# Kernel optimization log

Hardware: AMD Instinct MI355X
Metric: run time of the kernel (lower is better)

Reference implementation:

```python
import jax, jax.numpy as jnp
import numpy as np

D = 1024
H = 16
DH = D // H  # 64
EPS_LN = 1e-5
CONF_MIN = 1e-6


def sparsemax(z):
    """Sparsemax along the last axis (Martins & Astudillo 2016)."""
    K = z.shape[-1]
    z_sorted = jnp.flip(jnp.sort(z, axis=-1), axis=-1)          # descending
    cssv = jnp.cumsum(z_sorted, axis=-1)                        # cumulative sums
    r = jnp.arange(1, K + 1, dtype=z.dtype)                     # 1..K
    support = (1.0 + r * z_sorted) > cssv                       # bool mask
    k = jnp.sum(support, axis=-1, keepdims=True)                # support size
    tau = (jnp.take_along_axis(cssv, k.astype(jnp.int32) - 1, axis=-1) - 1.0) / k.astype(z.dtype)
    return jnp.maximum(z - tau, 0.0)


def setup_inputs() -> dict:
    key = jax.random.key(0)
    ks = jax.random.split(key, 16)
    B, P, K = 8, 512, 16
    s = 0.02
    return {
        "cell_query": jax.random.normal(ks[0], (B, D), jnp.float32),
        "gene_facets": jax.random.normal(ks[1], (B, P, K, D), jnp.float32),
        "confidence": jax.random.uniform(ks[2], (B, P, K), jnp.float32),
        "wq": jax.random.normal(ks[3], (D, D), jnp.float32) * s,
        "bq": jnp.zeros((D,), jnp.float32),
        "wk": jax.random.normal(ks[4], (D, D), jnp.float32) * s,
        "bk": jnp.zeros((D,), jnp.float32),
        "wv": jax.random.normal(ks[5], (D, D), jnp.float32) * s,
        "bv": jnp.zeros((D,), jnp.float32),
        "wo": jax.random.normal(ks[6], (D, D), jnp.float32) * s,
        "bo": jnp.zeros((D,), jnp.float32),
        "gamma": jnp.ones((D,), jnp.float32),
        "beta": jnp.zeros((D,), jnp.float32),
    }


def reference(cell_query, gene_facets, confidence,
              wq, bq, wk, bk, wv, bv, wo, bo, gamma, beta):
    B = gene_facets.shape[0]
    P = gene_facets.shape[1]
    Kf = gene_facets.shape[2]

    # Projections (torch Linear: x @ W^T + b; here weights stored already transposed as (D,D))
    Q = (cell_query @ wq + bq).reshape(B, H, DH)                       # (B,H,d)
    Kp = (gene_facets @ wk + bk).reshape(B, P, Kf, H, DH)              # (B,P,K,H,d)
    Vp = (gene_facets @ wv + bv).reshape(B, P, Kf, H, DH)              # (B,P,K,H,d)

    # scores: (B,P,H,K)
    scores = jnp.einsum('bhd,bpkhd->bphk', Q, Kp) / jnp.sqrt(jnp.asarray(DH, Q.dtype))
    conf_bias = jnp.log(jnp.clip(confidence, CONF_MIN))                # (B,P,K)
    scores = scores + conf_bias[:, :, None, :]

    alpha = sparsemax(scores)                                          # (B,P,H,K), dropout_p=0 -> identity

    out = jnp.einsum('bphk,bpkhd->bphd', alpha, Vp).reshape(B, P, D)
    out = out @ wo + bo

    # LayerNorm over last dim
    mu = jnp.mean(out, axis=-1, keepdims=True)
    var = jnp.mean((out - mu) ** 2, axis=-1, keepdims=True)
    out = (out - mu) * jax.lax.rsqrt(var + EPS_LN) * gamma + beta
    return out, alpha
```

## Files before the change

### kernel.cpp

```cpp
#include <hip/hip_runtime.h>


typedef float f32x4 __attribute__((ext_vector_type(4)));
typedef short s16x4 __attribute__((ext_vector_type(4)));
typedef short s16x8 __attribute__((ext_vector_type(8)));

__device__ __forceinline__ unsigned short f2bf(float f) {
  unsigned u = __builtin_bit_cast(unsigned, f);
  u = (u + 0x7FFFu + ((u >> 16) & 1u)) >> 16;
  return (unsigned short)u;
}

__device__ __forceinline__ s16x8 pack8(s16x4 lo, s16x4 hi) {
  s16x8 r;
  r[0] = lo[0]; r[1] = lo[1]; r[2] = lo[2]; r[3] = lo[3];
  r[4] = hi[0]; r[5] = hi[1]; r[6] = hi[2]; r[7] = hi[3];
  return r;
}

__global__ __launch_bounds__(256) void k_trans(
    const float* __restrict__ wv, const float* __restrict__ wo,
    unsigned short* __restrict__ wvt, unsigned short* __restrict__ wot) {
  __shared__ float ts[64][65];
  int bid = blockIdx.x;
  const float* src = (bid < 256) ? wv : wo;
  unsigned short* dst = (bid < 256) ? wvt : wot;
  int tile = bid & 255;
  int er = (tile >> 4) << 6;
  int cb = (tile & 15) << 6;
  int t = threadIdx.x;
  int r = t >> 2, c0 = (t & 3) << 4;
#pragma unroll
  for (int j = 0; j < 16; j += 4) {
    f32x4 v = *(const f32x4*)&src[(long)(er + r) * 1024 + cb + c0 + j];
    ts[r][c0 + j + 0] = v[0];
    ts[r][c0 + j + 1] = v[1];
    ts[r][c0 + j + 2] = v[2];
    ts[r][c0 + j + 3] = v[3];
  }
  __syncthreads();
  s16x8 o0, o1;
#pragma unroll
  for (int j = 0; j < 8; ++j) o0[j] = (short)f2bf(ts[c0 + j][r]);
#pragma unroll
  for (int j = 0; j < 8; ++j) o1[j] = (short)f2bf(ts[c0 + 8 + j][r]);
  long ob = (long)(cb + r) * 1024 + er + c0;
  *(s16x8*)&dst[ob] = o0;
  *(s16x8*)&dst[ob + 8] = o1;
}

__global__ __launch_bounds__(256) void k_qpart(
    const float* __restrict__ cq, const float* __restrict__ wq,
    float* __restrict__ qpart) {
  int eq = blockIdx.x, b = blockIdx.y, t = threadIdx.x;
  int d0 = t << 2;
  f32x4 acc = {0.f, 0.f, 0.f, 0.f};
#pragma unroll 4
  for (int i = 0; i < 64; ++i) {
    int e = (eq << 6) + i;
    float c = cq[(b << 10) + e];
    f32x4 w = *(const f32x4*)&wq[(long)e * 1024 + d0];
    acc += w * c;
  }
  *(f32x4*)&qpart[(long)((b << 4) + eq) * 1024 + d0] = acc;
}

__global__ __launch_bounds__(256) void k_wtilde(
    const float* __restrict__ wk, const float* __restrict__ bk,
    const float* __restrict__ bq, const float* __restrict__ qpart,
    unsigned short* __restrict__ wt, float* __restrict__ cvec) {
  __shared__ float Qs[16][68];
  int et = blockIdx.x, b = blockIdx.y, t = threadIdx.x;
#pragma unroll
  for (int j = 0; j < 4; ++j) {
    int d = t + (j << 8);
    float s = bq[d];
    for (int q = 0; q < 16; ++q) s += qpart[(long)((b << 4) + q) * 1024 + d];
    Qs[d >> 6][d & 63] = s;
  }
  __syncthreads();
  int h = t & 15, el = t >> 4;
#pragma unroll
  for (int ii = 0; ii < 8; ++ii) {
    int e = (et << 7) + (ii << 4) + el;
    const float* wr = &wk[(long)e * 1024 + (h << 6)];
    float s = 0.f;
#pragma unroll
    for (int d = 0; d < 64; d += 4) {
      f32x4 w = *(const f32x4*)&wr[d];
      s += w[0] * Qs[h][d] + w[1] * Qs[h][d + 1] + w[2] * Qs[h][d + 2] + w[3] * Qs[h][d + 3];
    }
    wt[(long)((b << 4) + h) * 1024 + e] = f2bf(s);
  }
  if (et == 0 && t < 16) {
    float s = 0.f;
    for (int d = 0; d < 64; ++d) s += bk[(t << 6) + d] * Qs[t][d];
    cvec[(b << 4) + t] = s;
  }
}

#define GSTR 1028
__global__ __launch_bounds__(256, 2) void k_scores(
    const float* __restrict__ G, const float* __restrict__ conf,
    const unsigned short* __restrict__ wt, const float* __restrict__ cvec,
    float* __restrict__ alpha_out, unsigned short* __restrict__ gbar, int b0) {
  __shared__ short smem[33408];
  __shared__ float fsm[1040];
  short* Gs = smem;
  short* Ws = smem + 16 * GSTR;
  short* As = smem + 32 * GSTR;
  float* ps = fsm;
  float* lc = fsm + 1024;

  int t = threadIdx.x;
  int lane = t & 63, w = t >> 6;
  int bp = blockIdx.x;
  long gbp = (long)b0 * 512 + bp;
  int b = (int)(gbp >> 9);
  const float* Grow = G + gbp * 16384;
  const unsigned short* wtb = wt + (long)b * 16384;

#pragma unroll
  for (int it = 0; it < 8; ++it) {
    int flat = (it << 11) + (t << 3);
    s16x8 v = *(const s16x8*)&wtb[flat];
    short* dst = &Ws[(flat >> 10) * GSTR + (flat & 1023)];
    *(s16x4*)dst = (s16x4){v[0], v[1], v[2], v[3]};
    *(s16x4*)(dst + 4) = (s16x4){v[4], v[5], v[6], v[7]};
  }
  if (t < 32) {
    short* base = (t < 16) ? Gs : Ws;
    *(s16x4*)&base[(t & 15) * GSTR + 1024] = (s16x4){0, 0, 0, 0};
  }
  if (t < 16) lc[t] = logf(fmaxf(conf[gbp * 16 + t], 1e-6f));

#pragma unroll
  for (int k = 0; k < 16; ++k) {
    f32x4 g = *(const f32x4*)&Grow[(k << 10) + (t << 2)];
    s16x4 h4;
    h4[0] = (short)f2bf(g[0]); h4[1] = (short)f2bf(g[1]);
    h4[2] = (short)f2bf(g[2]); h4[3] = (short)f2bf(g[3]);
    *(s16x4*)&Gs[k * GSTR + (t << 2)] = h4;
  }
  __syncthreads();

  int l15 = lane & 15, g4 = lane >> 4;
  f32x4 sc = {0.f, 0.f, 0.f, 0.f};
#pragma unroll
  for (int i = 0; i < 8; ++i) {
    int eb = (w << 8) + (i << 5) + (g4 << 3);
    int off = l15 * GSTR + eb;
    s16x8 avf = pack8(*(const s16x4*)&Ws[off], *(const s16x4*)&Ws[off + 4]);
    s16x8 bvf = pack8(*(const s16x4*)&Gs[off], *(const s16x4*)&Gs[off + 4]);
    sc = __builtin_amdgcn_mfma_f32_16x16x32_bf16(avf, bvf, sc, 0, 0, 0);
  }
#pragma unroll
  for (int r = 0; r < 4; ++r)
    ps[(w << 8) + ((g4 << 2) + r) * 16 + l15] = sc[r];
  __syncthreads();

  int h = t >> 4, k = t & 15;
  float z = (ps[h * 16 + k] + ps[256 + h * 16 + k] + ps[512 + h * 16 + k] +
             ps[768 + h * 16 + k] + cvec[b * 16 + h]) * 0.125f + lc[k];
  float v = z;
#pragma unroll
  for (int kk = 2; kk <= 16; kk <<= 1) {
#pragma unroll
    for (int j = kk >> 1; j > 0; j >>= 1) {
      float o = __shfl_xor(v, j, 64);
      bool dirDesc = ((l15 & kk) == 0);
      bool takeMax = (((l15 & j) == 0) == dirDesc);
      v = takeMax ? fmaxf(v, o) : fminf(v, o);
    }
  }
  float cs = v;
#pragma unroll
  for (int d = 1; d < 16; d <<= 1) {
    float o = __shfl_up(cs, (unsigned)d, 16);
    if (l15 >= d) cs += o;
  }
  bool sup = (1.0f + (float)(l15 + 1) * v) > cs;
  unsigned long long m = __ballot(sup);
  int gb16 = lane & 48;
  int ksup = (int)__popcll((m >> gb16) & 0xFFFFull);
  float csk = __shfl(cs, ksup - 1, 16);
  float tau = (csk - 1.0f) / (float)ksup;
  float a = fmaxf(z - tau, 0.0f);
  alpha_out[((gbp << 4) + h) * 16 + k] = a;
  As[(h << 5) + k] = (short)f2bf(a);
  As[(h << 5) + 16 + k] = 0;
  __syncthreads();

  s16x8 ab = *(const s16x8*)&As[(l15 << 5) + (g4 << 3)];
  unsigned short* gbo = gbar + ((long)bp << 14);
#pragma unroll 4
  for (int i = 0; i < 16; ++i) {
    int ebase = ((w << 4) + i) << 4;
    int eA = ebase + l15;
    s16x8 aa;
#pragma unroll
    for (int j = 0; j < 8; ++j) aa[j] = Gs[((g4 << 3) + j) * GSTR + eA];
    f32x4 d2 = __builtin_amdgcn_mfma_f32_16x16x32_bf16(
        aa, ab, (f32x4){0.f, 0.f, 0.f, 0.f}, 0, 0, 0);
    s16x4 o4;
    o4[0] = (short)f2bf(d2[0]); o4[1] = (short)f2bf(d2[1]);
    o4[2] = (short)f2bf(d2[2]); o4[3] = (short)f2bf(d2[3]);
    *(s16x4*)&gbo[(l15 << 10) + ebase + (g4 << 2)] = o4;
  }
}

__global__ __launch_bounds__(256) void k_av(
    const unsigned short* __restrict__ gbar, const unsigned short* __restrict__ wvt,
    const float* __restrict__ bv, unsigned short* __restrict__ av, int b0) {
  __shared__ short Asm[64 * 40];
  __shared__ short Bsm[64 * 40];
  int tile = blockIdx.x, h = blockIdx.y, t = threadIdx.x;
  int lane = t & 63, w = t >> 6;
  int wm = w >> 1, wn = w & 1;
  int l15 = lane & 15, g4 = lane >> 4;
  f32x4 acc[2][2] = {};
  int lr = t >> 2, ls = (t & 3) << 3;
  const unsigned short* Ar = gbar + ((long)(tile * 64 + lr)) * 16384 + h * 1024;
  const unsigned short* Br = wvt + ((long)((h << 6) + lr)) * 1024;
  s16x8 a8 = *(const s16x8*)&Ar[ls];
  s16x8 b8 = *(const s16x8*)&Br[ls];
  for (int kb = 0; kb < 32; ++kb) {
    __syncthreads();
    *(s16x8*)&Asm[lr * 40 + ls] = a8;
    *(s16x8*)&Bsm[lr * 40 + ls] = b8;
    if (kb + 1 < 32) {
      a8 = *(const s16x8*)&Ar[((kb + 1) << 5) + ls];
      b8 = *(const s16x8*)&Br[((kb + 1) << 5) + ls];
    }
    __syncthreads();
    s16x8 afr[2], bfr[2];
#pragma unroll
    for (int im = 0; im < 2; ++im)
      afr[im] = *(const s16x8*)&Asm[(wm * 32 + im * 16 + l15) * 40 + (g4 << 3)];
#pragma unroll
    for (int in = 0; in < 2; ++in)
      bfr[in] = *(const s16x8*)&Bsm[(wn * 32 + in * 16 + l15) * 40 + (g4 << 3)];
#pragma unroll
    for (int im = 0; im < 2; ++im)
#pragma unroll
      for (int in = 0; in < 2; ++in)
        acc[im][in] = __builtin_amdgcn_mfma_f32_16x16x32_bf16(afr[im], bfr[in], acc[im][in], 0, 0, 0);
  }
#pragma unroll
  for (int in = 0; in < 2; ++in) {
    int colg = (h << 6) + wn * 32 + in * 16 + l15;
    float bvv = bv[colg];
#pragma unroll
    for (int im = 0; im < 2; ++im) {
      long rowg = (long)b0 * 512 + tile * 64 + wm * 32 + im * 16 + (g4 << 2);
#pragma unroll
      for (int r = 0; r < 4; ++r)
        av[(rowg + r) * 1024 + colg] = f2bf(acc[im][in][r] + bvv);
    }
  }
}

__global__ __launch_bounds__(256) void k_out(
    const unsigned short* __restrict__ av, const unsigned short* __restrict__ wot,
    const float* __restrict__ bo, float* __restrict__ y) {
  __shared__ short Asm[128 * 40];
  __shared__ short Bsm[128 * 40];
  int mt = blockIdx.x, nt = blockIdx.y, t = threadIdx.x;
  int lane = t & 63, w = t >> 6;
  int wm = w >> 1, wn = w & 1;
  int l15 = lane & 15, g4 = lane >> 4;
  f32x4 acc[4][4] = {};
  int lr = t >> 1, ls = (t & 1) << 4;
  const unsigned short* Ar = av + ((long)(mt * 128 + lr)) * 1024;
  const unsigned short* Br = wot + ((long)(nt * 128 + lr)) * 1024;
  s16x8 a0 = *(const s16x8*)&Ar[ls];
  s16x8 a1 = *(const s16x8*)&Ar[ls + 8];
  s16x8 b0 = *(const s16x8*)&Br[ls];
  s16x8 b1 = *(const s16x8*)&Br[ls + 8];
  for (int kb = 0; kb < 32; ++kb) {
    __syncthreads();
    short* pa = &Asm[lr * 40 + ls];
    *(s16x8*)pa = a0; *(s16x8*)(pa + 8) = a1;
    short* pb = &Bsm[lr * 40 + ls];
    *(s16x8*)pb = b0; *(s16x8*)(pb + 8) = b1;
    if (kb + 1 < 32) {
      a0 = *(const s16x8*)&Ar[((kb + 1) << 5) + ls];
      a1 = *(const s16x8*)&Ar[((kb + 1) << 5) + ls + 8];
      b0 = *(const s16x8*)&Br[((kb + 1) << 5) + ls];
      b1 = *(const s16x8*)&Br[((kb + 1) << 5) + ls + 8];
    }
    __syncthreads();
    s16x8 afr[4], bfr[4];
#pragma unroll
    for (int im = 0; im < 4; ++im)
      afr[im] = *(const s16x8*)&Asm[(wm * 64 + im * 16 + l15) * 40 + (g4 << 3)];
#pragma unroll
    for (int in = 0; in < 4; ++in)
      bfr[in] = *(const s16x8*)&Bsm[(wn * 64 + in * 16 + l15) * 40 + (g4 << 3)];
#pragma unroll
    for (int im = 0; im < 4; ++im)
#pragma unroll
      for (int in = 0; in < 4; ++in)
        acc[im][in] = __builtin_amdgcn_mfma_f32_16x16x32_bf16(afr[im], bfr[in], acc[im][in], 0, 0, 0);
  }
#pragma unroll
  for (int in = 0; in < 4; ++in) {
    int colg = nt * 128 + wn * 64 + in * 16 + l15;
    float bov = bo[colg];
#pragma unroll
    for (int im = 0; im < 4; ++im) {
      long rowg = mt * 128 + wm * 64 + im * 16 + (g4 << 2);
#pragma unroll
      for (int r = 0; r < 4; ++r)
        y[(rowg + r) * 1024 + colg] = acc[im][in][r] + bov;
    }
  }
}

__global__ __launch_bounds__(256) void k_ln(
    float* __restrict__ y, const float* __restrict__ gamma,
    const float* __restrict__ beta) {
  int row = (blockIdx.x << 2) + (threadIdx.x >> 6);
  int lane = threadIdx.x & 63;
  float* yr = y + ((long)row << 10);
  f32x4 v[4];
  float s = 0.f, s2 = 0.f;
#pragma unroll
  for (int j = 0; j < 4; ++j) {
    v[j] = *(const f32x4*)&yr[(lane << 2) + (j << 8)];
#pragma unroll
    for (int q = 0; q < 4; ++q) { s += v[j][q]; s2 += v[j][q] * v[j][q]; }
  }
#pragma unroll
  for (int d = 1; d < 64; d <<= 1) {
    s += __shfl_xor(s, d, 64);
    s2 += __shfl_xor(s2, d, 64);
  }
  float mu = s * (1.0f / 1024.0f);
  float var = s2 * (1.0f / 1024.0f) - mu * mu;
  float rs = rsqrtf(var + 1e-5f);
#pragma unroll
  for (int j = 0; j < 4; ++j) {
    int f0 = (lane << 2) + (j << 8);
    f32x4 gm = *(const f32x4*)&gamma[f0];
    f32x4 bt = *(const f32x4*)&beta[f0];
    f32x4 o;
#pragma unroll
    for (int q = 0; q < 4; ++q) o[q] = (v[j][q] - mu) * rs * gm[q] + bt[q];
    *(f32x4*)&yr[f0] = o;
  }
}

extern "C" void kernel_launch(void* const* d_in, const int* in_sizes, int n_in,
                              void* d_out, int out_size, void* d_ws, size_t ws_size,
                              hipStream_t stream) {
  (void)in_sizes; (void)n_in; (void)out_size;
  const float* cq    = (const float*)d_in[0];
  const float* G     = (const float*)d_in[1];
  const float* conf  = (const float*)d_in[2];
  const float* wq    = (const float*)d_in[3];
  const float* bq    = (const float*)d_in[4];
  const float* wk    = (const float*)d_in[5];
  const float* bk    = (const float*)d_in[6];
  const float* wv    = (const float*)d_in[7];
  const float* bv    = (const float*)d_in[8];
  const float* wo    = (const float*)d_in[9];
  const float* bo    = (const float*)d_in[10];
  const float* gamma = (const float*)d_in[11];
  const float* beta  = (const float*)d_in[12];

  float* y = (float*)d_out;
  float* alpha = y + 4194304;

  char* p = (char*)d_ws;
  float* qpart = (float*)p;                 p += 8L * 16 * 1024 * 4;
  float* cvec  = (float*)p;                 p += 1024;
  unsigned short* wt   = (unsigned short*)p; p += 8L * 16 * 1024 * 2;
  unsigned short* wvt  = (unsigned short*)p; p += 1024L * 1024 * 2;
  unsigned short* wot  = (unsigned short*)p; p += 1024L * 1024 * 2;
  unsigned short* av   = (unsigned short*)p; p += 4096L * 1024 * 2;
  unsigned short* gbar = (unsigned short*)p;
  size_t used = (size_t)(p - (char*)d_ws);
  size_t per_b = 512L * 16 * 1024 * 2;
  int nb = 1;
  if (ws_size >= used + 8 * per_b) nb = 8;
  else if (ws_size >= used + 4 * per_b) nb = 4;
  else if (ws_size >= used + 2 * per_b) nb = 2;

  hipLaunchKernelGGL(k_trans, dim3(512), dim3(256), 0, stream, wv, wo, wvt, wot);
  hipLaunchKernelGGL(k_qpart, dim3(16, 8), dim3(256), 0, stream, cq, wq, qpart);
  hipLaunchKernelGGL(k_wtilde, dim3(8, 8), dim3(256), 0, stream, wk, bk, bq, qpart, wt, cvec);
  for (int c = 0; c < 8; c += nb) {
    hipLaunchKernelGGL(k_scores, dim3(nb * 512), dim3(256), 0, stream,
                       G, conf, wt, cvec, alpha, gbar, c);
    hipLaunchKernelGGL(k_av, dim3(nb * 8, 16), dim3(256), 0, stream,
                       gbar, wvt, bv, av, c);
  }
  hipLaunchKernelGGL(k_out, dim3(32, 8), dim3(256), 0, stream, av, wot, bo, y);
  hipLaunchKernelGGL(k_ln, dim3(1024), dim3(256), 0, stream, y, gamma, beta);
}
```

Baseline: 232.2 us.

## Transpose gbar to head-major, stage transposed G tile, enlarge k_av tiles

k_scores now builds a transposed bf16 copy of the G tile in shared memory, so the second MFMA reads contiguous vectors instead of eight strided scalar LDS loads. It reads the W-tilde fragments straight from global memory rather than staging them in LDS. gbar is written head-major (head stride passed as a parameter) so k_av reads contiguous rows, and k_av now uses 128-row tiles, launching half as many blocks. k_qpart computes all 8 batches in one block per weight slice, so wq is read once instead of eight times. The extra LDS for Gt raises shared-memory use, which may cut k_scores occupancy.

```diff
diff --git a/kernel.cpp b/kernel.cpp
--- a/kernel.cpp
+++ b/kernel.cpp
@@ -52,17 +52,18 @@
 __global__ __launch_bounds__(256) void k_qpart(
     const float* __restrict__ cq, const float* __restrict__ wq,
     float* __restrict__ qpart) {
-  int eq = blockIdx.x, b = blockIdx.y, t = threadIdx.x;
+  int eq = blockIdx.x, t = threadIdx.x;
   int d0 = t << 2;
-  f32x4 acc = {0.f, 0.f, 0.f, 0.f};
-#pragma unroll 4
+  f32x4 acc[8] = {};
   for (int i = 0; i < 64; ++i) {
     int e = (eq << 6) + i;
-    float c = cq[(b << 10) + e];
     f32x4 w = *(const f32x4*)&wq[(long)e * 1024 + d0];
-    acc += w * c;
-  }
-  *(f32x4*)&qpart[(long)((b << 4) + eq) * 1024 + d0] = acc;
+#pragma unroll
+    for (int b = 0; b < 8; ++b) acc[b] += w * cq[(b << 10) + e];
+  }
+#pragma unroll
+  for (int b = 0; b < 8; ++b)
+    *(f32x4*)&qpart[(long)((b << 4) + eq) * 1024 + d0] = acc[b];
 }
 
 __global__ __launch_bounds__(256) void k_wtilde(
@@ -100,20 +101,21 @@
 }
 
 #define GSTR 1028
+#define TSTR 20
 __global__ __launch_bounds__(256, 2) void k_scores(
     const float* __restrict__ G, const float* __restrict__ conf,
     const unsigned short* __restrict__ wt, const float* __restrict__ cvec,
-    float* __restrict__ alpha_out, unsigned short* __restrict__ gbar, int b0) {
-  __shared__ short smem[33408];
-  __shared__ float fsm[1040];
-  short* Gs = smem;
-  short* Ws = smem + 16 * GSTR;
-  short* As = smem + 32 * GSTR;
-  float* ps = fsm;
-  float* lc = fsm + 1024;
+    float* __restrict__ alpha_out, unsigned short* __restrict__ gbar,
+    int b0, int hstride) {
+  __shared__ short Gs[16 * GSTR];
+  __shared__ short Gt[1024 * TSTR];
+  __shared__ short As[16 * 32];
+  __shared__ float ps[1024];
+  __shared__ float lc[16];
 
   int t = threadIdx.x;
   int lane = t & 63, w = t >> 6;
+  int l15 = lane & 15, g4 = lane >> 4;
   int bp = blockIdx.x;
   long gbp = (long)b0 * 512 + bp;
   int b = (int)(gbp >> 9);
@@ -121,138 +123,147 @@
   const unsigned short* wtb = wt + (long)b * 16384;
 
 #pragma unroll
-  for (int it = 0; it < 8; ++it) {
-    int flat = (it << 11) + (t << 3);
-    s16x8 v = *(const s16x8*)&wtb[flat];
-    short* dst = &Ws[(flat >> 10) * GSTR + (flat & 1023)];
-    *(s16x4*)dst = (s16x4){v[0], v[1], v[2], v[3]};
-    *(s16x4*)(dst + 4) = (s16x4){v[4], v[5], v[6], v[7]};
-  }
-  if (t < 32) {
-    short* base = (t < 16) ? Gs : Ws;
-    *(s16x4*)&base[(t & 15) * GSTR + 1024] = (s16x4){0, 0, 0, 0};
+  for (int half = 0; half < 2; ++half) {
+    s16x4 col[8];
+#pragma unroll
+    for (int j = 0; j < 8; ++j) {
+      int k = (half << 3) + j;
+      f32x4 g = *(const f32x4*)&Grow[(k << 10) + (t << 2)];
+      s16x4 h4;
+      h4[0] = (short)f2bf(g[0]); h4[1] = (short)f2bf(g[1]);
+      h4[2] = (short)f2bf(g[2]); h4[3] = (short)f2bf(g[3]);
+      *(s16x4*)&Gs[k * GSTR + (t << 2)] = h4;
+      col[j] = h4;
+    }
+#pragma unroll
+    for (int q = 0; q < 4; ++q) {
+      int e = (t << 2) + q;
+      s16x4 lo, hi;
+      lo[0] = col[0][q]; lo[1] = col[1][q]; lo[2] = col[2][q]; lo[3] = col[3][q];
+      hi[0] = col[4][q]; hi[1] = col[5][q]; hi[2] = col[6][q]; hi[3] = col[7][q];
+      *(s16x4*)&Gt[e * TSTR + (half << 3)] = lo;
+      *(s16x4*)&Gt[e * TSTR + (half << 3) + 4] = hi;
+    }
   }
   if (t < 16) lc[t] = logf(fmaxf(conf[gbp * 16 + t], 1e-6f));
-
-#pragma unroll
-  for (int k = 0; k < 16; ++k) {
-    f32x4 g = *(const f32x4*)&Grow[(k << 10) + (t << 2)];
-    s16x4 h4;
-    h4[0] = (short)f2bf(g[0]); h4[1] = (short)f2bf(g[1]);
-    h4[2] = (short)f2bf(g[2]); h4[3] = (short)f2bf(g[3]);
-    *(s16x4*)&Gs[k * GSTR + (t << 2)] = h4;
-  }
   __syncthreads();
 
-  int l15 = lane & 15, g4 = lane >> 4;
   f32x4 sc = {0.f, 0.f, 0.f, 0.f};
 #pragma unroll
   for (int i = 0; i < 8; ++i) {
-    int eb = (w << 8) + (i << 5) + (g4 << 3);
-    int off = l15 * GSTR + eb;
-    s16x8 avf = pack8(*(const s16x4*)&Ws[off], *(const s16x4*)&Ws[off + 4]);
-    s16x8 bvf = pack8(*(const s16x4*)&Gs[off], *(const s16x4*)&Gs[off + 4]);
-    sc = __builtin_amdgcn_mfma_f32_16x16x32_bf16(avf, bvf, sc, 0, 0, 0);
+    int e0 = (w << 8) + (i << 5) + (g4 << 3);
+    s16x8 af = *(const s16x8*)&wtb[l15 * 1024 + e0];
+    int off = l15 * GSTR + e0;
+    s16x8 bf = pack8(*(const s16x4*)&Gs[off], *(const s16x4*)&Gs[off + 4]);
+    sc = __builtin_amdgcn_mfma_f32_16x16x32_bf16(af, bf, sc, 0, 0, 0);
   }
 #pragma unroll
   for (int r = 0; r < 4; ++r)
     ps[(w << 8) + ((g4 << 2) + r) * 16 + l15] = sc[r];
   __syncthreads();
 
-  int h = t >> 4, k = t & 15;
-  float z = (ps[h * 16 + k] + ps[256 + h * 16 + k] + ps[512 + h * 16 + k] +
-             ps[768 + h * 16 + k] + cvec[b * 16 + h]) * 0.125f + lc[k];
-  float v = z;
-#pragma unroll
-  for (int kk = 2; kk <= 16; kk <<= 1) {
-#pragma unroll
-    for (int j = kk >> 1; j > 0; j >>= 1) {
-      float o = __shfl_xor(v, j, 64);
-      bool dirDesc = ((l15 & kk) == 0);
-      bool takeMax = (((l15 & j) == 0) == dirDesc);
-      v = takeMax ? fmaxf(v, o) : fminf(v, o);
-    }
-  }
-  float cs = v;
-#pragma unroll
-  for (int d = 1; d < 16; d <<= 1) {
-    float o = __shfl_up(cs, (unsigned)d, 16);
-    if (l15 >= d) cs += o;
-  }
-  bool sup = (1.0f + (float)(l15 + 1) * v) > cs;
-  unsigned long long m = __ballot(sup);
-  int gb16 = lane & 48;
-  int ksup = (int)__popcll((m >> gb16) & 0xFFFFull);
-  float csk = __shfl(cs, ksup - 1, 16);
-  float tau = (csk - 1.0f) / (float)ksup;
-  float a = fmaxf(z - tau, 0.0f);
-  alpha_out[((gbp << 4) + h) * 16 + k] = a;
-  As[(h << 5) + k] = (short)f2bf(a);
-  As[(h << 5) + 16 + k] = 0;
+  {
+    int h = t >> 4, k = t & 15;
+    float z = (ps[h * 16 + k] + ps[256 + h * 16 + k] + ps[512 + h * 16 + k] +
+               ps[768 + h * 16 + k] + cvec[b * 16 + h]) * 0.125f + lc[k];
+    float v = z;
+#pragma unroll
+    for (int kk = 2; kk <= 16; kk <<= 1) {
+#pragma unroll
+      for (int j = kk >> 1; j > 0; j >>= 1) {
+        float o = __shfl_xor(v, j, 64);
+        bool dirDesc = ((l15 & kk) == 0);
+        bool takeMax = (((l15 & j) == 0) == dirDesc);
+        v = takeMax ? fmaxf(v, o) : fminf(v, o);
+      }
+    }
+    float cs = v;
+#pragma unroll
+    for (int d = 1; d < 16; d <<= 1) {
+      float o = __shfl_up(cs, (unsigned)d, 16);
+      if (l15 >= d) cs += o;
+    }
+    bool sup = (1.0f + (float)(l15 + 1) * v) > cs;
+    unsigned long long m = __ballot(sup);
+    int gb16 = lane & 48;
+    int ksup = (int)__popcll((m >> gb16) & 0xFFFFull);
+    float csk = __shfl(cs, ksup - 1, 16);
+    float tau = (csk - 1.0f) / (float)ksup;
+    float a = fmaxf(z - tau, 0.0f);
+    alpha_out[((gbp << 4) + h) * 16 + k] = a;
+    As[(h << 5) + k] = (short)f2bf(a);
+    As[(h << 5) + 16 + k] = 0;
+  }
   __syncthreads();
 
   s16x8 ab = *(const s16x8*)&As[(l15 << 5) + (g4 << 3)];
-  unsigned short* gbo = gbar + ((long)bp << 14);
 #pragma unroll 4
   for (int i = 0; i < 16; ++i) {
     int ebase = ((w << 4) + i) << 4;
-    int eA = ebase + l15;
-    s16x8 aa;
-#pragma unroll
-    for (int j = 0; j < 8; ++j) aa[j] = Gs[((g4 << 3) + j) * GSTR + eA];
+    int ro = (ebase + l15) * TSTR + ((g4 & 1) << 3);
+    s16x8 aa = pack8(*(const s16x4*)&Gt[ro], *(const s16x4*)&Gt[ro + 4]);
     f32x4 d2 = __builtin_amdgcn_mfma_f32_16x16x32_bf16(
         aa, ab, (f32x4){0.f, 0.f, 0.f, 0.f}, 0, 0, 0);
     s16x4 o4;
     o4[0] = (short)f2bf(d2[0]); o4[1] = (short)f2bf(d2[1]);
     o4[2] = (short)f2bf(d2[2]); o4[3] = (short)f2bf(d2[3]);
-    *(s16x4*)&gbo[(l15 << 10) + ebase + (g4 << 2)] = o4;
+    *(s16x4*)&gbar[(long)l15 * hstride + (long)bp * 1024 + ebase + (g4 << 2)] = o4;
   }
 }
 
 __global__ __launch_bounds__(256) void k_av(
     const unsigned short* __restrict__ gbar, const unsigned short* __restrict__ wvt,
-    const float* __restrict__ bv, unsigned short* __restrict__ av, int b0) {
-  __shared__ short Asm[64 * 40];
+    const float* __restrict__ bv, unsigned short* __restrict__ av,
+    int b0, int hstride) {
+  __shared__ short Asm[128 * 40];
   __shared__ short Bsm[64 * 40];
-  int tile = blockIdx.x, h = blockIdx.y, t = threadIdx.x;
+  int t = threadIdx.x;
   int lane = t & 63, w = t >> 6;
+  int l15 = lane & 15, g4 = lane >> 4;
   int wm = w >> 1, wn = w & 1;
-  int l15 = lane & 15, g4 = lane >> 4;
-  f32x4 acc[2][2] = {};
-  int lr = t >> 2, ls = (t & 3) << 3;
-  const unsigned short* Ar = gbar + ((long)(tile * 64 + lr)) * 16384 + h * 1024;
-  const unsigned short* Br = wvt + ((long)((h << 6) + lr)) * 1024;
-  s16x8 a8 = *(const s16x8*)&Ar[ls];
-  s16x8 b8 = *(const s16x8*)&Br[ls];
+  int tile = blockIdx.x, h = blockIdx.y;
+  const unsigned short* Ab = gbar + (long)h * hstride + (long)tile * 128 * 1024;
+  const unsigned short* Bb = wvt + (long)(h << 6) * 1024;
+  int ar = t >> 1, ac = (t & 1) << 4;
+  int br = t >> 2, bc = (t & 3) << 3;
+  const unsigned short* Arp = Ab + (long)ar * 1024 + ac;
+  const unsigned short* Brp = Bb + (long)br * 1024 + bc;
+  s16x8 a0 = *(const s16x8*)&Arp[0];
+  s16x8 a1 = *(const s16x8*)&Arp[8];
+  s16x8 b8 = *(const s16x8*)&Brp[0];
+  f32x4 acc[4][2] = {};
   for (int kb = 0; kb < 32; ++kb) {
     __syncthreads();
-    *(s16x8*)&Asm[lr * 40 + ls] = a8;
-    *(s16x8*)&Bsm[lr * 40 + ls] = b8;
+    short* pa = &Asm[ar * 40 + ac];
+    *(s16x8*)pa = a0; *(s16x8*)(pa + 8) = a1;
+    *(s16x8*)&Bsm[br * 40 + bc] = b8;
     if (kb + 1 < 32) {
-      a8 = *(const s16x8*)&Ar[((kb + 1) << 5) + ls];
-      b8 = *(const s16x8*)&Br[((kb + 1) << 5) + ls];
+      a0 = *(const s16x8*)&Arp[((kb + 1) << 5)];
+      a1 = *(const s16x8*)&Arp[((kb + 1) << 5) + 8];
+      b8 = *(const s16x8*)&Brp[((kb + 1) << 5)];
     }
     __syncthreads();
-    s16x8 afr[2], bfr[2];
-#pragma unroll
-    for (int im = 0; im < 2; ++im)
-      afr[im] = *(const s16x8*)&Asm[(wm * 32 + im * 16 + l15) * 40 + (g4 << 3)];
+    s16x8 afr[4], bfr[2];
+#pragma unroll
+    for (int im = 0; im < 4; ++im)
+      afr[im] = *(const s16x8*)&Asm[(wm * 64 + im * 16 + l15) * 40 + (g4 << 3)];
 #pragma unroll
     for (int in = 0; in < 2; ++in)
       bfr[in] = *(const s16x8*)&Bsm[(wn * 32 + in * 16 + l15) * 40 + (g4 << 3)];
 #pragma unroll
-    for (int im = 0; im < 2; ++im)
+    for (int im = 0; im < 4; ++im)
 #pragma unroll
       for (int in = 0; in < 2; ++in)
         acc[im][in] = __builtin_amdgcn_mfma_f32_16x16x32_bf16(afr[im], bfr[in], acc[im][in], 0, 0, 0);
   }
+  long grow0 = (long)b0 * 512 + (long)tile * 128 + wm * 64 + (g4 << 2);
 #pragma unroll
   for (int in = 0; in < 2; ++in) {
     int colg = (h << 6) + wn * 32 + in * 16 + l15;
     float bvv = bv[colg];
 #pragma unroll
-    for (int im = 0; im < 2; ++im) {
-      long rowg = (long)b0 * 512 + tile * 64 + wm * 32 + im * 16 + (g4 << 2);
+    for (int im = 0; im < 4; ++im) {
+      long rowg = grow0 + im * 16;
 #pragma unroll
       for (int r = 0; r < 4; ++r)
         av[(rowg + r) * 1024 + colg] = f2bf(acc[im][in][r] + bvv);
@@ -373,8 +384,8 @@
   float* alpha = y + 4194304;
 
   char* p = (char*)d_ws;
-  float* qpart = (float*)p;                 p += 8L * 16 * 1024 * 4;
-  float* cvec  = (float*)p;                 p += 1024;
+  float* qpart = (float*)p;                  p += 8L * 16 * 1024 * 4;
+  float* cvec  = (float*)p;                  p += 1024;
   unsigned short* wt   = (unsigned short*)p; p += 8L * 16 * 1024 * 2;
   unsigned short* wvt  = (unsigned short*)p; p += 1024L * 1024 * 2;
   unsigned short* wot  = (unsigned short*)p; p += 1024L * 1024 * 2;
@@ -386,15 +397,16 @@
   if (ws_size >= used + 8 * per_b) nb = 8;
   else if (ws_size >= used + 4 * per_b) nb = 4;
   else if (ws_size >= used + 2 * per_b) nb = 2;
+  int hstride = nb * 512 * 1024;
 
   hipLaunchKernelGGL(k_trans, dim3(512), dim3(256), 0, stream, wv, wo, wvt, wot);
-  hipLaunchKernelGGL(k_qpart, dim3(16, 8), dim3(256), 0, stream, cq, wq, qpart);
+  hipLaunchKernelGGL(k_qpart, dim3(16), dim3(256), 0, stream, cq, wq, qpart);
   hipLaunchKernelGGL(k_wtilde, dim3(8, 8), dim3(256), 0, stream, wk, bk, bq, qpart, wt, cvec);
   for (int c = 0; c < 8; c += nb) {
     hipLaunchKernelGGL(k_scores, dim3(nb * 512), dim3(256), 0, stream,
-                       G, conf, wt, cvec, alpha, gbar, c);
-    hipLaunchKernelGGL(k_av, dim3(nb * 8, 16), dim3(256), 0, stream,
-                       gbar, wvt, bv, av, c);
+                       G, conf, wt, cvec, alpha, gbar, c, hstride);
+    hipLaunchKernelGGL(k_av, dim3(nb * 4, 16), dim3(256), 0, stream,
+                       gbar, wvt, bv, av, c, hstride);
   }
   hipLaunchKernelGGL(k_out, dim3(32, 8), dim3(256), 0, stream, av, wot, bo, y);
   hipLaunchKernelGGL(k_ln, dim3(1024), dim3(256), 0, stream, y, gamma, beta);
```

After: 232.6 us. No clear change (+0.2%).
